# Performance work log

Hardware: AMD Instinct MI355X
Metric: run time of the kernel (lower is better)

## Reference

```python
import jax, jax.numpy as jnp
import numpy as np

T, D_IN, D_OUT, L, R = 8192, 4096, 4096, 16, 16


def setup_inputs() -> dict:
    key = jax.random.key(0)
    ks = jax.random.split(key, 7)
    x = jax.random.normal(ks[0], (T, D_IN), dtype=jnp.float32)
    W = jax.random.normal(ks[1], (D_OUT, D_IN), dtype=jnp.float32) / np.sqrt(D_IN)
    base_bias = jax.random.normal(ks[2], (D_OUT,), dtype=jnp.float32)
    # stacked LoRA weights (squeezed over the dummy dim-1 in the torch code)
    lora_a = jax.random.normal(ks[3], (L, R, D_IN), dtype=jnp.float32) / np.sqrt(D_IN)
    lora_b = jax.random.normal(ks[4], (L, D_OUT, R), dtype=jnp.float32) / np.sqrt(R)
    bias_stacked = jax.random.normal(ks[5], (L, D_OUT), dtype=jnp.float32)
    # per-token adapter index in [-1, L); -1 means "no LoRA"
    indices = jax.random.randint(ks[6], (T,), -1, L, dtype=jnp.int32)
    return {"x": x, "W": W, "base_bias": base_bias, "lora_a": lora_a,
            "lora_b": lora_b, "bias_stacked": bias_stacked, "indices": indices}


def reference(x, W, base_bias, lora_a, lora_b, bias_stacked, indices):
    num_loras = lora_a.shape[0]
    # base dense GEMM + base bias (ReplicatedLinear.quant_method.apply)
    out = x @ W.T + base_bias  # [T, D_OUT]
    # one_hot gives an all-zero row for indices == -1, matching the masking
    # in apply_bias and the no-op semantics of add_lora for unmapped tokens.
    onehot = jax.nn.one_hot(indices, num_loras, dtype=x.dtype)  # [T, L]
    # per-adapter bias gather-scatter (apply_bias)
    out = out + onehot @ bias_stacked  # [T, D_OUT]
    # SGMV-style LoRA: shrink with A, expand with B, scatter-add into out.
    shrunk_all = jnp.einsum('td,lrd->ltr', x, lora_a)        # [L, T, R]
    shrunk = jnp.einsum('tl,ltr->tr', onehot, shrunk_all)    # [T, R] per-token
    masked = onehot[:, :, None] * shrunk[:, None, :]         # [T, L, R]
    out = out + jnp.einsum('tlr,lor->to', masked, lora_b)    # [T, D_OUT]
    return out
```

## Files before the change

kernel.cpp:

```cpp
#include <hip/hip_runtime.h>
#include <hip/hip_bf16.h>
#include <stdint.h>

typedef unsigned short u16;
typedef unsigned int u32;

#define T_TOK 8192
#define DIN   4096
#define DOUT  4096
#define NL    16
#define NR    16
#define KX    4096
#define K2    4416
#define NKT   69
#define GITERS 34

typedef __attribute__((ext_vector_type(8))) __bf16 bf16x8;
typedef __attribute__((ext_vector_type(4))) float  f32x4;

__device__ __forceinline__ u32 bf16rne(float f) {
    u32 x = __float_as_uint(f);
    return (x + 0x7FFFu + ((x >> 16) & 1u)) >> 16;
}
__device__ __forceinline__ u32 pack2(float a, float b) {
    return bf16rne(a) | (bf16rne(b) << 16);
}

__global__ void pack_mats(const float* __restrict__ x, const float* __restrict__ W,
                          u16* __restrict__ Abf, u16* __restrict__ Bbf) {
    const int total = (T_TOK + DOUT) * (DIN / 8);
    for (int i = blockIdx.x * blockDim.x + threadIdx.x; i < total;
         i += gridDim.x * blockDim.x) {
        int row = i >> 9;
        int c8  = (i & 511) << 3;
        const float* src;
        u16* dst;
        if (row < T_TOK) { src = x + (size_t)row * DIN; dst = Abf + (size_t)row * K2; }
        else { src = W + (size_t)(row - T_TOK) * DIN; dst = Bbf + (size_t)(row - T_TOK) * K2; }
        const float4* s = (const float4*)(src + c8);
        float4 f0 = s[0], f1 = s[1];
        uint4 u;
        u.x = pack2(f0.x, f0.y); u.y = pack2(f0.z, f0.w);
        u.z = pack2(f1.x, f1.y); u.w = pack2(f1.z, f1.w);
        *(uint4*)(dst + c8) = u;
    }
}

#define NBEX (DOUT * 320)
__global__ void pack_small(const float* __restrict__ lora_b,
                           const float* __restrict__ base_bias,
                           const float* __restrict__ bias_st,
                           const float* __restrict__ la,
                           u16* __restrict__ Bbf, u16* __restrict__ Aabf) {
    const int total = NBEX + NL * NR * DIN / 8;
    for (int i = blockIdx.x * blockDim.x + threadIdx.x; i < total;
         i += gridDim.x * blockDim.x) {
        if (i < NBEX) {
            int o = i / 320;
            int j = i - o * 320;
            float v = 0.f;
            if (j < 256) {
                int l = j >> 4, r = j & 15;
                v = lora_b[((size_t)l * DOUT + o) * NR + r];
            } else if (j == 256) {
                v = base_bias[o];
            } else if (j < 273) {
                v = bias_st[(size_t)(j - 257) * DOUT + o];
            }
            Bbf[(size_t)o * K2 + KX + j] = (u16)bf16rne(v);
        } else {
            int c8 = (i - NBEX) << 3;
            const float4* s = (const float4*)(la + c8);
            float4 f0 = s[0], f1 = s[1];
            uint4 u;
            u.x = pack2(f0.x, f0.y); u.y = pack2(f0.z, f0.w);
            u.z = pack2(f1.x, f1.y); u.w = pack2(f1.z, f1.w);
            *(uint4*)(Aabf + c8) = u;
        }
    }
}

__global__ __launch_bounds__(512) void zfill_kernel(const u16* __restrict__ Axr,
                                                    const u16* __restrict__ La,
                                                    const int* __restrict__ idx,
                                                    u16* __restrict__ Abf) {
    __shared__ u16 sX[2][64 * 64];
    __shared__ u16 sL[2][128 * 64];
    const int tid  = threadIdx.x;
    const int lane = tid & 63, wid = tid >> 6;
    const int wr = wid >> 2, wc = wid & 3;
    const int lrow = lane & 15;
    const int klo  = (lane >> 4) << 4;
    const int sxr  = (lrow & 7) << 4;
    const int kxb[2] = { klo ^ sxr, (64 + klo) ^ sxr };

    const int bt = blockIdx.x >> 1;
    const int nh = blockIdx.x & 1;

    const int r0 = tid >> 3;
    const int c4 = (tid & 7) ^ (r0 & 7);
    const u16* pX = Axr + (size_t)(bt * 64 + r0) * K2 + c4 * 8;
    const u16* pL = La + (size_t)(nh * 128 + r0) * DIN + c4 * 8;
    const u16* pL2 = La + (size_t)(nh * 128 + 64 + r0) * DIN + c4 * 8;

    f32x4 acc[2][2];
#pragma unroll
    for (int m = 0; m < 2; ++m)
#pragma unroll
        for (int n = 0; n < 2; ++n) { f32x4 z = {0.f,0.f,0.f,0.f}; acc[m][n] = z; }

#define STAGEZ(buf, kt)                                                                \
  do {                                                                                 \
    __builtin_amdgcn_global_load_lds(                                                  \
      (const __attribute__((address_space(1))) u32*)(pX + (size_t)(kt) * 64),          \
      (__attribute__((address_space(3))) u32*)(&sX[buf][tid * 8]), 16, 0, 0);          \
    __builtin_amdgcn_global_load_lds(                                                  \
      (const __attribute__((address_space(1))) u32*)(pL + (size_t)(kt) * 64),          \
      (__attribute__((address_space(3))) u32*)(&sL[buf][tid * 8]), 16, 0, 0);          \
    __builtin_amdgcn_global_load_lds(                                                  \
      (const __attribute__((address_space(1))) u32*)(pL2 + (size_t)(kt) * 64),         \
      (__attribute__((address_space(3))) u32*)(&sL[buf][4096 + tid * 8]), 16, 0, 0);   \
  } while (0)

    STAGEZ(0, 0);
    for (int kt = 0; kt < 64; ++kt) {
        const int cur = kt & 1;
        if (kt < 63) {
            STAGEZ(cur ^ 1, kt + 1);
            asm volatile("s_waitcnt vmcnt(3)" ::: "memory");
        } else {
            asm volatile("s_waitcnt vmcnt(0)" ::: "memory");
        }
        __builtin_amdgcn_sched_barrier(0);
        __builtin_amdgcn_s_barrier();
        __builtin_amdgcn_sched_barrier(0);
        const char* sx = (const char*)sX[cur];
        const char* sl = (const char*)sL[cur];
        bf16x8 a[2][2], b[2][2];
#pragma unroll
        for (int m = 0; m < 2; ++m)
#pragma unroll
            for (int kk = 0; kk < 2; ++kk)
                a[m][kk] = *(const bf16x8*)(sx + (wr * 32 + m * 16 + lrow) * 128 + kxb[kk]);
#pragma unroll
        for (int n = 0; n < 2; ++n)
#pragma unroll
            for (int kk = 0; kk < 2; ++kk)
                b[n][kk] = *(const bf16x8*)(sl + (wc * 32 + n * 16 + lrow) * 128 + kxb[kk]);
#pragma unroll
        for (int m = 0; m < 2; ++m)
#pragma unroll
            for (int n = 0; n < 2; ++n)
#pragma unroll
                for (int kk = 0; kk < 2; ++kk)
                    acc[m][n] = __builtin_amdgcn_mfma_f32_16x16x32_bf16(
                        a[m][kk], b[n][kk], acc[m][n], 0, 0, 0);
        __builtin_amdgcn_sched_barrier(0);
        __builtin_amdgcn_s_barrier();
        __builtin_amdgcn_sched_barrier(0);
    }

#pragma unroll
    for (int m = 0; m < 2; ++m) {
#pragma unroll
        for (int rg = 0; rg < 4; ++rg) {
            int tl = wr * 32 + m * 16 + ((lane >> 4) << 2) + rg;
            int t  = bt * 64 + tl;
            int l  = idx[t];
#pragma unroll
            for (int n = 0; n < 2; ++n) {
                int col = nh * 128 + wc * 32 + n * 16 + (lane & 15);
                u16 v = ((col >> 4) == l) ? (u16)bf16rne(acc[m][n][rg]) : (u16)0;
                Abf[(size_t)t * K2 + KX + col] = v;
            }
        }
    }
    if (nh == 0) {
        int tl = tid >> 3, c8 = (tid & 7) * 8;
        int t = bt * 64 + tl;
        int l = idx[t];
        u32 w[4];
#pragma unroll
        for (int q = 0; q < 4; ++q) {
            int c0 = KX + 256 + c8 + 2 * q;
            u32 v0 = (c0 == 4352 || (l >= 0 && c0 == 4353 + l)) ? 0x3F80u : 0u;
            int c1 = c0 + 1;
            u32 v1 = (c1 == 4352 || (l >= 0 && c1 == 4353 + l)) ? 0x3F80u : 0u;
            w[q] = v0 | (v1 << 16);
        }
        *(uint4*)(Abf + (size_t)t * K2 + KX + 256 + c8) = *(uint4*)w;
    }
}


#define SBAR() __builtin_amdgcn_sched_barrier(0)
#define HWBAR() __builtin_amdgcn_s_barrier()
#define PHASE_BAR() do { SBAR(); HWBAR(); SBAR(); } while (0)
#define VMCNT4() asm volatile("s_waitcnt vmcnt(4)" ::: "memory")
#define VMCNT0() asm volatile("s_waitcnt vmcnt(0)" ::: "memory")

#define STAGE(ptr, h, buf, seg, kt)                                                   \
  do { if ((kt) < NKT) {                                                              \
    __builtin_amdgcn_global_load_lds(                                                 \
      (const __attribute__((address_space(1))) u32*)((ptr) + (size_t)((h)*128 + 0)*K2 + (size_t)(kt)*64),  \
      (__attribute__((address_space(3))) u32*)(lds16 + ((((buf)*4+(seg))<<13) + tid*8)), 16, 0, 0);        \
    __builtin_amdgcn_global_load_lds(                                                 \
      (const __attribute__((address_space(1))) u32*)((ptr) + (size_t)((h)*128 + 64)*K2 + (size_t)(kt)*64), \
      (__attribute__((address_space(3))) u32*)(lds16 + ((((buf)*4+(seg))<<13) + tid*8 + 4096)), 16, 0, 0); \
  } } while (0)

#define RD_AH(buf, mh, aa)                                                            \
  { _Pragma("unroll") for (int mm = 0; mm < 4; ++mm)                                  \
    _Pragma("unroll") for (int kk = 0; kk < 2; ++kk)                                  \
      aa[mm][kk] = *(const bf16x8*)(smem + (((buf)*4 + wr) << 14) + lrow*128          \
          + (mh)*8192 + mm*2048 + kxb[kk]); }

#define RD_BH(buf, nh, bf)                                                            \
  { _Pragma("unroll") for (int nn = 0; nn < 2; ++nn)                                  \
    _Pragma("unroll") for (int kk = 0; kk < 2; ++kk)                                  \
      bf[nn][kk] = *(const bf16x8*)(smem + (((buf)*4 + 2 + (wc>>1)) << 14)            \
          + ((wc&1)*64 + lrow)*128 + ((nh)*2+nn)*2048 + kxb[kk]); }

#define MMQ(mh, nh, aa, bf)                                                           \
  { __builtin_amdgcn_s_setprio(1);                                                    \
    _Pragma("unroll") for (int mm = 0; mm < 4; ++mm)                                  \
    _Pragma("unroll") for (int nn = 0; nn < 2; ++nn)                                  \
    _Pragma("unroll") for (int kk = 0; kk < 2; ++kk)                                  \
      acc[(mh)*4+mm][(nh)*2+nn] = __builtin_amdgcn_mfma_f32_16x16x32_bf16(            \
          aa[mm][kk], bf[nn][kk], acc[(mh)*4+mm][(nh)*2+nn], 0, 0, 0);                \
    __builtin_amdgcn_s_setprio(0); }

__global__ __launch_bounds__(512, 2) void gemm_kernel(const u16* __restrict__ A,
                                                      const u16* __restrict__ B,
                                                      float* __restrict__ C) {
    __shared__ u16 lds16[65536];
    const char* smem = (const char*)lds16;

    const int tid  = threadIdx.x;
    const int lane = tid & 63, wid = tid >> 6;
    const int wr = wid >> 2, wc = wid & 3;
    const int lrow = lane & 15;
    const int klo  = (lane >> 4) << 4;
    const int sx   = (lrow & 7) << 4;
    const int kxb[2] = { klo ^ sx, (64 + klo) ^ sx };

    const int wg  = blockIdx.x;
    const int swz = (wg & 7) * 64 + (wg >> 3);
    const int bm = swz >> 4;
    const int bn = swz & 15;

    const int r0  = tid >> 3;
    const int sc4 = (tid & 7) ^ (r0 & 7);
    const u16* pA = A + (size_t)(bm * 256 + r0) * K2 + sc4 * 8;
    const u16* pB = B + (size_t)(bn * 256 + r0) * K2 + sc4 * 8;

    f32x4 acc[8][4];
#pragma unroll
    for (int m = 0; m < 8; ++m)
#pragma unroll
        for (int n = 0; n < 4; ++n) { f32x4 z = {0.f,0.f,0.f,0.f}; acc[m][n] = z; }
    bf16x8 a0[4][2], a1[4][2], bA[2][2], bB[2][2];

    STAGE(pA, 0, 0, 0, 0); STAGE(pA, 1, 0, 1, 0);
    STAGE(pB, 0, 0, 2, 0); STAGE(pB, 1, 0, 3, 0);
    STAGE(pA, 0, 1, 0, 1); STAGE(pB, 0, 1, 2, 1);
    VMCNT4();
    PHASE_BAR();

    for (int i = 0; i < GITERS; ++i) {
        const int kO = 2 * i + 1, kE2 = 2 * i + 2, kO2 = 2 * i + 3;
        RD_AH(0, 0, a0); RD_BH(0, 0, bA); RD_BH(0, 1, bB);
        STAGE(pA, 1, 1, 1, kO); STAGE(pB, 1, 1, 3, kO);
        MMQ(0, 0, a0, bA); MMQ(0, 1, a0, bB);
        PHASE_BAR();
        RD_AH(0, 1, a1);
        STAGE(pA, 0, 0, 0, kE2); STAGE(pB, 0, 0, 2, kE2);
        MMQ(1, 0, a1, bA); MMQ(1, 1, a1, bB);
        VMCNT4();
        PHASE_BAR();
        RD_AH(1, 0, a0); RD_BH(1, 0, bA); RD_BH(1, 1, bB);
        STAGE(pA, 1, 0, 1, kE2); STAGE(pB, 1, 0, 3, kE2);
        MMQ(0, 0, a0, bA); MMQ(0, 1, a0, bB);
        PHASE_BAR();
        RD_AH(1, 1, a1);
        STAGE(pA, 0, 1, 0, kO2); STAGE(pB, 0, 1, 2, kO2);
        MMQ(1, 0, a1, bA); MMQ(1, 1, a1, bB);
        VMCNT4();
        PHASE_BAR();
    }

    VMCNT0();
    PHASE_BAR();
    RD_AH(0, 0, a0); RD_AH(0, 1, a1); RD_BH(0, 0, bA); RD_BH(0, 1, bB);
    MMQ(0, 0, a0, bA); MMQ(1, 0, a1, bA); MMQ(0, 1, a0, bB); MMQ(1, 1, a1, bB);

    const int crow0 = bm * 256 + wr * 128 + ((lane >> 4) << 2);
    const int ccol0 = bn * 256 + wc * 64 + (lane & 15);
#pragma unroll
    for (int m = 0; m < 8; ++m)
#pragma unroll
        for (int n = 0; n < 4; ++n)
#pragma unroll
            for (int rg = 0; rg < 4; ++rg)
                C[(size_t)(crow0 + m * 16 + rg) * DOUT + ccol0 + n * 16] = acc[m][n][rg];
}


extern "C" void kernel_launch(void* const* d_in, const int* in_sizes, int n_in,
                              void* d_out, int out_size, void* d_ws, size_t ws_size,
                              hipStream_t stream) {
    const float* x         = (const float*)d_in[0];
    const float* W         = (const float*)d_in[1];
    const float* base_bias = (const float*)d_in[2];
    const float* lora_a    = (const float*)d_in[3];
    const float* lora_b    = (const float*)d_in[4];
    const float* bias_st   = (const float*)d_in[5];
    const int*   indices   = (const int*)d_in[6];
    float* out = (float*)d_out;

    u16* Abf  = (u16*)d_ws;
    u16* Bbf  = Abf + (size_t)T_TOK * K2;
    u16* Aabf = Bbf + (size_t)DOUT * K2;

    pack_mats<<<6144, 256, 0, stream>>>(x, W, Abf, Bbf);
    pack_small<<<1536, 256, 0, stream>>>(lora_b, base_bias, bias_st, lora_a, Bbf, Aabf);
    zfill_kernel<<<256, 512, 0, stream>>>(Abf, Aabf, indices, Abf);
    gemm_kernel<<<512, 512, 0, stream>>>(Abf, Bbf, out);
    (void)in_sizes; (void)n_in; (void)out_size; (void)ws_size;
}
```

Before: 346.5 us.

## Move biases into GEMM epilogue, shrink K extension, merge pack kernels

The base bias and per-adapter bias leave the augmented K dimension and are now added in the GEMM epilogue from fp32 inputs, gathered through the token index. The GEMM K loop therefore drops its trailing tile (68 tiles instead of 69). The two packing kernels become one launch that packs lora_b with vectorised stores. The zfill shrink kernel switches to smaller 256-thread blocks over more column slices for better occupancy. The epilogue gains an index load and a scattered bias read per row, in exchange for less K work and one fewer launch.

```diff
diff --git a/kernel.cpp b/kernel.cpp
--- a/kernel.cpp
+++ b/kernel.cpp
@@ -12,7 +12,7 @@
 #define NR    16
 #define KX    4096
 #define K2    4416
-#define NKT   69
+#define NKT   68
 #define GITERS 34
 
 typedef __attribute__((ext_vector_type(8))) __bf16 bf16x8;
@@ -26,82 +26,65 @@
     return bf16rne(a) | (bf16rne(b) << 16);
 }
 
-__global__ void pack_mats(const float* __restrict__ x, const float* __restrict__ W,
-                          u16* __restrict__ Abf, u16* __restrict__ Bbf) {
-    const int total = (T_TOK + DOUT) * (DIN / 8);
+#define NCHUNK_XW ((T_TOK + DOUT) * 512)
+#define NCHUNK_BX (DOUT * 32)
+#define NCHUNK_LA (NL * NR * DIN / 8)
+__global__ void pack_all(const float* __restrict__ x, const float* __restrict__ W,
+                         const float* __restrict__ lora_b, const float* __restrict__ la,
+                         u16* __restrict__ Abf, u16* __restrict__ Bbf,
+                         u16* __restrict__ Aabf) {
+    const int total = NCHUNK_XW + NCHUNK_BX + NCHUNK_LA;
     for (int i = blockIdx.x * blockDim.x + threadIdx.x; i < total;
          i += gridDim.x * blockDim.x) {
-        int row = i >> 9;
-        int c8  = (i & 511) << 3;
-        const float* src;
-        u16* dst;
-        if (row < T_TOK) { src = x + (size_t)row * DIN; dst = Abf + (size_t)row * K2; }
-        else { src = W + (size_t)(row - T_TOK) * DIN; dst = Bbf + (size_t)(row - T_TOK) * K2; }
-        const float4* s = (const float4*)(src + c8);
-        float4 f0 = s[0], f1 = s[1];
+        const float* s;
+        u16* d;
+        if (i < NCHUNK_XW) {
+            int row = i >> 9;
+            int c8  = (i & 511) << 3;
+            if (row < T_TOK) { s = x + (size_t)row * DIN + c8; d = Abf + (size_t)row * K2 + c8; }
+            else { s = W + (size_t)(row - T_TOK) * DIN + c8; d = Bbf + (size_t)(row - T_TOK) * K2 + c8; }
+        } else if (i < NCHUNK_XW + NCHUNK_BX) {
+            int j = i - NCHUNK_XW;
+            int o = j >> 5;
+            int c8 = (j & 31) << 3;
+            int l = c8 >> 4, rb = c8 & 15;
+            s = lora_b + ((size_t)l * DOUT + o) * NR + rb;
+            d = Bbf + (size_t)o * K2 + KX + c8;
+        } else {
+            int c8 = (i - NCHUNK_XW - NCHUNK_BX) << 3;
+            s = la + c8;
+            d = Aabf + c8;
+        }
+        const float4* s4 = (const float4*)s;
+        float4 f0 = s4[0], f1 = s4[1];
         uint4 u;
         u.x = pack2(f0.x, f0.y); u.y = pack2(f0.z, f0.w);
         u.z = pack2(f1.x, f1.y); u.w = pack2(f1.z, f1.w);
-        *(uint4*)(dst + c8) = u;
-    }
-}
-
-#define NBEX (DOUT * 320)
-__global__ void pack_small(const float* __restrict__ lora_b,
-                           const float* __restrict__ base_bias,
-                           const float* __restrict__ bias_st,
-                           const float* __restrict__ la,
-                           u16* __restrict__ Bbf, u16* __restrict__ Aabf) {
-    const int total = NBEX + NL * NR * DIN / 8;
-    for (int i = blockIdx.x * blockDim.x + threadIdx.x; i < total;
-         i += gridDim.x * blockDim.x) {
-        if (i < NBEX) {
-            int o = i / 320;
-            int j = i - o * 320;
-            float v = 0.f;
-            if (j < 256) {
-                int l = j >> 4, r = j & 15;
-                v = lora_b[((size_t)l * DOUT + o) * NR + r];
-            } else if (j == 256) {
-                v = base_bias[o];
-            } else if (j < 273) {
-                v = bias_st[(size_t)(j - 257) * DOUT + o];
-            }
-            Bbf[(size_t)o * K2 + KX + j] = (u16)bf16rne(v);
-        } else {
-            int c8 = (i - NBEX) << 3;
-            const float4* s = (const float4*)(la + c8);
-            float4 f0 = s[0], f1 = s[1];
-            uint4 u;
-            u.x = pack2(f0.x, f0.y); u.y = pack2(f0.z, f0.w);
-            u.z = pack2(f1.x, f1.y); u.w = pack2(f1.z, f1.w);
-            *(uint4*)(Aabf + c8) = u;
-        }
-    }
-}
-
-__global__ __launch_bounds__(512) void zfill_kernel(const u16* __restrict__ Axr,
+        *(uint4*)d = u;
+    }
+}
+
+__global__ __launch_bounds__(256) void zfill_kernel(const u16* __restrict__ Axr,
                                                     const u16* __restrict__ La,
                                                     const int* __restrict__ idx,
                                                     u16* __restrict__ Abf) {
     __shared__ u16 sX[2][64 * 64];
-    __shared__ u16 sL[2][128 * 64];
+    __shared__ u16 sL[2][64 * 64];
     const int tid  = threadIdx.x;
     const int lane = tid & 63, wid = tid >> 6;
-    const int wr = wid >> 2, wc = wid & 3;
+    const int wr = wid >> 1, wc = wid & 1;
     const int lrow = lane & 15;
     const int klo  = (lane >> 4) << 4;
     const int sxr  = (lrow & 7) << 4;
     const int kxb[2] = { klo ^ sxr, (64 + klo) ^ sxr };
 
-    const int bt = blockIdx.x >> 1;
-    const int nh = blockIdx.x & 1;
+    const int bt = blockIdx.x >> 2;
+    const int nh = blockIdx.x & 3;
 
     const int r0 = tid >> 3;
     const int c4 = (tid & 7) ^ (r0 & 7);
     const u16* pX = Axr + (size_t)(bt * 64 + r0) * K2 + c4 * 8;
-    const u16* pL = La + (size_t)(nh * 128 + r0) * DIN + c4 * 8;
-    const u16* pL2 = La + (size_t)(nh * 128 + 64 + r0) * DIN + c4 * 8;
+    const u16* pL = La + (size_t)(nh * 64 + r0) * DIN + c4 * 8;
 
     f32x4 acc[2][2];
 #pragma unroll
@@ -109,17 +92,20 @@
 #pragma unroll
         for (int n = 0; n < 2; ++n) { f32x4 z = {0.f,0.f,0.f,0.f}; acc[m][n] = z; }
 
-#define STAGEZ(buf, kt)                                                                \
-  do {                                                                                 \
-    __builtin_amdgcn_global_load_lds(                                                  \
-      (const __attribute__((address_space(1))) u32*)(pX + (size_t)(kt) * 64),          \
-      (__attribute__((address_space(3))) u32*)(&sX[buf][tid * 8]), 16, 0, 0);          \
-    __builtin_amdgcn_global_load_lds(                                                  \
-      (const __attribute__((address_space(1))) u32*)(pL + (size_t)(kt) * 64),          \
-      (__attribute__((address_space(3))) u32*)(&sL[buf][tid * 8]), 16, 0, 0);          \
-    __builtin_amdgcn_global_load_lds(                                                  \
-      (const __attribute__((address_space(1))) u32*)(pL2 + (size_t)(kt) * 64),         \
-      (__attribute__((address_space(3))) u32*)(&sL[buf][4096 + tid * 8]), 16, 0, 0);   \
+#define STAGEZ(buf, kt)                                                                 \
+  do {                                                                                  \
+    __builtin_amdgcn_global_load_lds(                                                   \
+      (const __attribute__((address_space(1))) u32*)(pX + (size_t)(kt) * 64),           \
+      (__attribute__((address_space(3))) u32*)(&sX[buf][tid * 8]), 16, 0, 0);           \
+    __builtin_amdgcn_global_load_lds(                                                   \
+      (const __attribute__((address_space(1))) u32*)(pX + (size_t)32 * K2 + (size_t)(kt) * 64),  \
+      (__attribute__((address_space(3))) u32*)(&sX[buf][2048 + tid * 8]), 16, 0, 0);    \
+    __builtin_amdgcn_global_load_lds(                                                   \
+      (const __attribute__((address_space(1))) u32*)(pL + (size_t)(kt) * 64),           \
+      (__attribute__((address_space(3))) u32*)(&sL[buf][tid * 8]), 16, 0, 0);           \
+    __builtin_amdgcn_global_load_lds(                                                   \
+      (const __attribute__((address_space(1))) u32*)(pL + (size_t)32 * DIN + (size_t)(kt) * 64), \
+      (__attribute__((address_space(3))) u32*)(&sL[buf][2048 + tid * 8]), 16, 0, 0);    \
   } while (0)
 
     STAGEZ(0, 0);
@@ -127,7 +113,7 @@
         const int cur = kt & 1;
         if (kt < 63) {
             STAGEZ(cur ^ 1, kt + 1);
-            asm volatile("s_waitcnt vmcnt(3)" ::: "memory");
+            asm volatile("s_waitcnt vmcnt(4)" ::: "memory");
         } else {
             asm volatile("s_waitcnt vmcnt(0)" ::: "memory");
         }
@@ -164,34 +150,17 @@
     for (int m = 0; m < 2; ++m) {
 #pragma unroll
         for (int rg = 0; rg < 4; ++rg) {
-            int tl = wr * 32 + m * 16 + ((lane >> 4) << 2) + rg;
-            int t  = bt * 64 + tl;
-            int l  = idx[t];
+            int t = bt * 64 + wr * 32 + m * 16 + ((lane >> 4) << 2) + rg;
+            int l = idx[t];
 #pragma unroll
             for (int n = 0; n < 2; ++n) {
-                int col = nh * 128 + wc * 32 + n * 16 + (lane & 15);
-                u16 v = ((col >> 4) == l) ? (u16)bf16rne(acc[m][n][rg]) : (u16)0;
-                Abf[(size_t)t * K2 + KX + col] = v;
+                int colr = nh * 64 + wc * 32 + n * 16 + (lane & 15);
+                u16 v = ((colr >> 4) == l) ? (u16)bf16rne(acc[m][n][rg]) : (u16)0;
+                Abf[(size_t)t * K2 + KX + colr] = v;
             }
         }
     }
-    if (nh == 0) {
-        int tl = tid >> 3, c8 = (tid & 7) * 8;
-        int t = bt * 64 + tl;
-        int l = idx[t];
-        u32 w[4];
-#pragma unroll
-        for (int q = 0; q < 4; ++q) {
-            int c0 = KX + 256 + c8 + 2 * q;
-            u32 v0 = (c0 == 4352 || (l >= 0 && c0 == 4353 + l)) ? 0x3F80u : 0u;
-            int c1 = c0 + 1;
-            u32 v1 = (c1 == 4352 || (l >= 0 && c1 == 4353 + l)) ? 0x3F80u : 0u;
-            w[q] = v0 | (v1 << 16);
-        }
-        *(uint4*)(Abf + (size_t)t * K2 + KX + 256 + c8) = *(uint4*)w;
-    }
-}
-
+}
 
 #define SBAR() __builtin_amdgcn_sched_barrier(0)
 #define HWBAR() __builtin_amdgcn_s_barrier()
@@ -232,6 +201,9 @@
 
 __global__ __launch_bounds__(512, 2) void gemm_kernel(const u16* __restrict__ A,
                                                       const u16* __restrict__ B,
+                                                      const float* __restrict__ base_bias,
+                                                      const float* __restrict__ bias_st,
+                                                      const int* __restrict__ gidx,
                                                       float* __restrict__ C) {
     __shared__ u16 lds16[65536];
     const char* smem = (const char*)lds16;
@@ -276,7 +248,7 @@
         RD_AH(0, 1, a1);
         STAGE(pA, 0, 0, 0, kE2); STAGE(pB, 0, 0, 2, kE2);
         MMQ(1, 0, a1, bA); MMQ(1, 1, a1, bB);
-        VMCNT4();
+        if (i == GITERS - 1) { VMCNT0(); } else { VMCNT4(); }
         PHASE_BAR();
         RD_AH(1, 0, a0); RD_BH(1, 0, bA); RD_BH(1, 1, bB);
         STAGE(pA, 1, 0, 1, kE2); STAGE(pB, 1, 0, 3, kE2);
@@ -289,20 +261,25 @@
         PHASE_BAR();
     }
 
-    VMCNT0();
-    PHASE_BAR();
-    RD_AH(0, 0, a0); RD_AH(0, 1, a1); RD_BH(0, 0, bA); RD_BH(0, 1, bB);
-    MMQ(0, 0, a0, bA); MMQ(1, 0, a1, bA); MMQ(0, 1, a0, bB); MMQ(1, 1, a1, bB);
-
     const int crow0 = bm * 256 + wr * 128 + ((lane >> 4) << 2);
     const int ccol0 = bn * 256 + wc * 64 + (lane & 15);
-#pragma unroll
-    for (int m = 0; m < 8; ++m)
-#pragma unroll
-        for (int n = 0; n < 4; ++n)
-#pragma unroll
-            for (int rg = 0; rg < 4; ++rg)
-                C[(size_t)(crow0 + m * 16 + rg) * DOUT + ccol0 + n * 16] = acc[m][n][rg];
+    float bb[4];
+#pragma unroll
+    for (int n = 0; n < 4; ++n) bb[n] = base_bias[ccol0 + n * 16];
+#pragma unroll
+    for (int m = 0; m < 8; ++m) {
+#pragma unroll
+        for (int rg = 0; rg < 4; ++rg) {
+            int row = crow0 + m * 16 + rg;
+            int l = gidx[row];
+#pragma unroll
+            for (int n = 0; n < 4; ++n) {
+                float v = acc[m][n][rg] + bb[n];
+                if (l >= 0) v += bias_st[(size_t)l * DOUT + ccol0 + n * 16];
+                C[(size_t)row * DOUT + ccol0 + n * 16] = v;
+            }
+        }
+    }
 }
 
 
@@ -322,9 +299,8 @@
     u16* Bbf  = Abf + (size_t)T_TOK * K2;
     u16* Aabf = Bbf + (size_t)DOUT * K2;
 
-    pack_mats<<<6144, 256, 0, stream>>>(x, W, Abf, Bbf);
-    pack_small<<<1536, 256, 0, stream>>>(lora_b, base_bias, bias_st, lora_a, Bbf, Aabf);
-    zfill_kernel<<<256, 512, 0, stream>>>(Abf, Aabf, indices, Abf);
-    gemm_kernel<<<512, 512, 0, stream>>>(Abf, Bbf, out);
+    pack_all<<<6144, 256, 0, stream>>>(x, W, lora_b, lora_a, Abf, Bbf, Aabf);
+    zfill_kernel<<<512, 256, 0, stream>>>(Abf, Aabf, indices, Abf);
+    gemm_kernel<<<512, 512, 0, stream>>>(Abf, Bbf, base_bias, bias_st, indices, out);
     (void)in_sizes; (void)n_in; (void)out_size; (void)ws_size;
 }
```

Result: no change. 343.3 us (-0.9%).
